# Optimization experiments

Measured on AMD Instinct MI355X. Metric: run time of the kernel, lower is better.

The kernel has to match this reference:

```python
import jax, jax.numpy as jnp
import numpy as np

EMBED = 128
HEADS = 32
HEAD_DIM = EMBED // HEADS  # 4
BATCH = 32
SEQ = 2048


def setup_inputs() -> dict:
    key = jax.random.key(0)
    ks = jax.random.split(key, 6)
    s = 1.0 / np.sqrt(EMBED)
    return {
        "x": jax.random.normal(ks[0], (BATCH, SEQ, EMBED), dtype=jnp.float32),
        # torch Linear weights are (out_features, in_features)
        "Wq": jax.random.uniform(ks[1], (EMBED, EMBED), jnp.float32, -s, s),
        "Wk": jax.random.uniform(ks[2], (EMBED, EMBED), jnp.float32, -s, s),
        "Wv": jax.random.uniform(ks[3], (EMBED, EMBED), jnp.float32, -s, s),
        "Wo": jax.random.uniform(ks[4], (EMBED, EMBED), jnp.float32, -s, s),
        "bo": jax.random.uniform(ks[5], (EMBED,), jnp.float32, -s, s),
    }


def reference(x, Wq, Wk, Wv, Wo, bo):
    b, s, e = x.shape
    h, d = HEADS, HEAD_DIM
    # projections (torch Linear: x @ W.T)
    q = (x @ Wq.T).reshape(b, s, h, d)
    k = (x @ Wk.T).reshape(b, s, h, d)
    v = (x @ Wv.T).reshape(b, s, h, d)
    # FAITHFUL to source: einsum 'bnqh,bnkh->bnqk' on (b, seq, heads, head_dim)
    # => n = seq position, q/k = HEADS. Attention is over the heads axis.
    scale = 1.0 / (float(d) ** 0.5)
    scores = jnp.einsum('bnqh,bnkh->bnqk', q, k) * scale  # (b, seq, heads, heads)
    attn = jax.nn.softmax(scores, axis=-1)
    attended = jnp.einsum('bnqk,bnkv->bnqv', attn, v).reshape(b, s, e)
    return attended @ Wo.T + bo
```

## Files before the change

kernel.cpp:

```cpp
#include <hip/hip_runtime.h>


#define TOKENS (32 * 2048)
#define E 128
#define NH 32
#define BT 16
#define THREADS 128
#define LPITCH 136

typedef __attribute__((ext_vector_type(4))) float f32x4;
typedef __attribute__((ext_vector_type(16))) float f32x16;
typedef __fp16 h8_t __attribute__((ext_vector_type(8)));

#if __has_builtin(__builtin_amdgcn_exp2f)
#define EXP2F __builtin_amdgcn_exp2f
#else
#define EXP2F exp2f
#endif

#if __has_builtin(__builtin_amdgcn_rcpf)
#define RCPF __builtin_amdgcn_rcpf
#else
#define RCPF(x) (1.0f / (x))
#endif

static __device__ __forceinline__ unsigned pk16(float a, float b) {
    return __builtin_bit_cast(unsigned, __builtin_amdgcn_cvt_pkrtz(a, b));
}

static __device__ __forceinline__ f32x16 zero16() {
    f32x16 z;
#pragma unroll
    for (int i = 0; i < 16; ++i) z[i] = 0.f;
    return z;
}

static __device__ __forceinline__ int vperm(int kh) {
    return ((kh >> 4) & 1) * 16 + ((kh >> 2) & 1) * 8 + ((kh >> 3) & 1) * 4 + (kh & 3);
}

__global__ void pack_w(const float* __restrict__ Wq, const float* __restrict__ Wk,
                       const float* __restrict__ Wv, const float* __restrict__ Wo,
                       __fp16* __restrict__ wpk) {
    int idx = blockIdx.x * blockDim.x + threadIdx.x;
    if (idx >= 4 * 8 * 4 * 64) return;
    int lane = idx & 63;
    int ks   = (idx >> 6) & 3;
    int nt   = (idx >> 8) & 7;
    int proj = idx >> 11;
    const float* W = (proj == 0) ? Wq : (proj == 1) ? Wk : (proj == 2) ? Wv : Wo;
    float scl = (proj == 1) ? 0.72134752044448170f : 1.0f;
    int c = lane & 15, g = lane >> 4;
    const float* src = W + (size_t)(nt * 16 + c) * E + ks * 32 + g * 8;
    __fp16* dst = wpk + (size_t)idx * 8;
#pragma unroll
    for (int j = 0; j < 8; ++j) dst[j] = (__fp16)(src[j] * scl);
}

__global__ __launch_bounds__(THREADS) void mha_fused(
        const float* __restrict__ x, const __fp16* __restrict__ wpk,
        const float* __restrict__ bo, float* __restrict__ out) {
    __shared__ __align__(16) __fp16 qs [BT * LPITCH];
    __shared__ __align__(16) __fp16 ksh[BT * LPITCH];
    __shared__ __align__(16) __fp16 vth[BT * LPITCH];

    const int tid  = threadIdx.x;
    const int wave = tid >> 6;
    const int lane = tid & 63;
    const int c = lane & 15, g = lane >> 4;
    const int bt0 = blockIdx.x * BT;

    {
        h8_t afrag[4];
        const float* xrow = x + (size_t)(bt0 + c) * E;
#pragma unroll
        for (int ks2 = 0; ks2 < 4; ++ks2) {
            const float* p = xrow + ks2 * 32 + g * 8;
            float4 v0 = *(const float4*)(p);
            float4 v1 = *(const float4*)(p + 4);
            uint4 au;
            au.x = pk16(v0.x, v0.y);
            au.y = pk16(v0.z, v0.w);
            au.z = pk16(v1.x, v1.y);
            au.w = pk16(v1.z, v1.w);
            afrag[ks2] = __builtin_bit_cast(h8_t, au);
        }

#pragma unroll
        for (int i = 0; i < 12; ++i) {
            int nc   = i * 2 + wave;
            int proj = i >> 2;
            int nt   = nc & 7;
            const __fp16* wb = wpk + ((size_t)((proj * 8 + nt) * 4) * 64 + lane) * 8;
            f32x4 acc = {0.f, 0.f, 0.f, 0.f};
#pragma unroll
            for (int ks2 = 0; ks2 < 4; ++ks2) {
                h8_t wf = *(const h8_t*)(wb + (size_t)ks2 * 64 * 8);
                acc = __builtin_amdgcn_mfma_f32_16x16x32_f16(wf, afrag[ks2], acc, 0, 0, 0);
            }
            if (proj < 2) {
                __fp16* dst = proj ? ksh : qs;
                uint2 st = make_uint2(pk16(acc[0], acc[1]), pk16(acc[2], acc[3]));
                *(uint2*)(dst + c * LPITCH + nt * 16 + g * 4) = st;
            } else {
                int vp = vperm(nt * 4 + g);
#pragma unroll
                for (int r2 = 0; r2 < 4; ++r2)
                    vth[c * LPITCH + r2 * 32 + vp] = (__fp16)acc[r2];
            }
        }
    }
    __syncthreads();

    {
        const int c32 = lane & 31;
        const int gg  = lane >> 5;
        const uint4 ONES4 = make_uint4(0x3C003C00u, 0x3C003C00u, 0x3C003C00u, 0x3C003C00u);
        const f32x16 z = zero16();
        const int tb = wave * 8;
#pragma unroll 1
        for (int pr = 0; pr < 4; ++pr) {
            const int t0 = tb + pr * 2, t1 = t0 + 1;
            const __fp16* v0r = vth + t0 * LPITCH;
            const __fp16* v1r = vth + t1 * LPITCH;

            uint4 ka0 = {0u,0u,0u,0u}, qa0 = {0u,0u,0u,0u};
            uint4 ka1 = {0u,0u,0u,0u}, qa1 = {0u,0u,0u,0u};
            if (gg == 0) {
                uint2 t;
                t = *(const uint2*)(ksh + t0 * LPITCH + c32 * 4); ka0.x = t.x; ka0.y = t.y;
                t = *(const uint2*)(qs  + t0 * LPITCH + c32 * 4); qa0.x = t.x; qa0.y = t.y;
                t = *(const uint2*)(ksh + t1 * LPITCH + c32 * 4); ka1.x = t.x; ka1.y = t.y;
                t = *(const uint2*)(qs  + t1 * LPITCH + c32 * 4); qa1.x = t.x; qa1.y = t.y;
            }
            uint4 va00 = *(const uint4*)(v0r + (c32 & 3) * 32 + gg * 8);
            uint4 va01 = *(const uint4*)(v0r + (c32 & 3) * 32 + 16 + gg * 8);
            uint4 va10 = *(const uint4*)(v1r + (c32 & 3) * 32 + gg * 8);
            uint4 va11 = *(const uint4*)(v1r + (c32 & 3) * 32 + 16 + gg * 8);
            if (c32 == 4) { va00 = ONES4; va01 = ONES4; va10 = ONES4; va11 = ONES4; }

            f32x16 sc0 = __builtin_amdgcn_mfma_f32_32x32x16_f16(
                __builtin_bit_cast(h8_t, ka0), __builtin_bit_cast(h8_t, qa0), z, 0, 0, 0);
            f32x16 sc1 = __builtin_amdgcn_mfma_f32_32x32x16_f16(
                __builtin_bit_cast(h8_t, ka1), __builtin_bit_cast(h8_t, qa1), z, 0, 0, 0);

            uint4 p00u, p01u, p10u, p11u;
            {
                float e[16];
#pragma unroll
                for (int r = 0; r < 16; ++r) e[r] = EXP2F(sc0[r]);
                p00u = make_uint4(pk16(e[0], e[1]),  pk16(e[2], e[3]),
                                  pk16(e[4], e[5]),  pk16(e[6], e[7]));
                p01u = make_uint4(pk16(e[8], e[9]),  pk16(e[10], e[11]),
                                  pk16(e[12], e[13]), pk16(e[14], e[15]));
            }
            {
                float e[16];
#pragma unroll
                for (int r = 0; r < 16; ++r) e[r] = EXP2F(sc1[r]);
                p10u = make_uint4(pk16(e[0], e[1]),  pk16(e[2], e[3]),
                                  pk16(e[4], e[5]),  pk16(e[6], e[7]));
                p11u = make_uint4(pk16(e[8], e[9]),  pk16(e[10], e[11]),
                                  pk16(e[12], e[13]), pk16(e[14], e[15]));
            }

            f32x16 pv0 = __builtin_amdgcn_mfma_f32_32x32x16_f16(
                __builtin_bit_cast(h8_t, va00), __builtin_bit_cast(h8_t, p00u), z, 0, 0, 0);
            pv0 = __builtin_amdgcn_mfma_f32_32x32x16_f16(
                __builtin_bit_cast(h8_t, va01), __builtin_bit_cast(h8_t, p01u), pv0, 0, 0, 0);
            f32x16 pv1 = __builtin_amdgcn_mfma_f32_32x32x16_f16(
                __builtin_bit_cast(h8_t, va10), __builtin_bit_cast(h8_t, p10u), z, 0, 0, 0);
            pv1 = __builtin_amdgcn_mfma_f32_32x32x16_f16(
                __builtin_bit_cast(h8_t, va11), __builtin_bit_cast(h8_t, p11u), pv1, 0, 0, 0);

            float s0 = __shfl(pv0[0], c32 + 32, 64);
            float s1 = __shfl(pv1[0], c32 + 32, 64);
            float r0 = RCPF(s0), r1 = RCPF(s1);
            if (lane < 32) {
                uint2 st0 = make_uint2(pk16(pv0[0] * r0, pv0[1] * r0),
                                       pk16(pv0[2] * r0, pv0[3] * r0));
                uint2 st1 = make_uint2(pk16(pv1[0] * r1, pv1[1] * r1),
                                       pk16(pv1[2] * r1, pv1[3] * r1));
                *(uint2*)(qs + t0 * LPITCH + c32 * 4) = st0;
                *(uint2*)(qs + t1 * LPITCH + c32 * 4) = st1;
            }
        }
    }
    __syncthreads();

    {
        h8_t af[4];
#pragma unroll
        for (int ks2 = 0; ks2 < 4; ++ks2) {
            af[ks2] = *(const h8_t*)(qs + c * LPITCH + ks2 * 32 + g * 8);
        }
#pragma unroll
        for (int i = 0; i < 4; ++i) {
            int nt = wave * 4 + i;
            const __fp16* wb = wpk + ((size_t)((3 * 8 + nt) * 4) * 64 + lane) * 8;
            f32x4 acc = {0.f, 0.f, 0.f, 0.f};
#pragma unroll
            for (int ks2 = 0; ks2 < 4; ++ks2) {
                h8_t b = *(const h8_t*)(wb + (size_t)ks2 * 64 * 8);
                acc = __builtin_amdgcn_mfma_f32_16x16x32_f16(b, af[ks2], acc, 0, 0, 0);
            }
            int col0 = nt * 16 + g * 4;
            float4 b4 = *(const float4*)(bo + col0);
            float4 st = make_float4(acc[0] + b4.x, acc[1] + b4.y,
                                    acc[2] + b4.z, acc[3] + b4.w);
            *(float4*)(out + (size_t)(bt0 + c) * E + col0) = st;
        }
    }
}

extern "C" void kernel_launch(void* const* d_in, const int* in_sizes, int n_in,
                              void* d_out, int out_size, void* d_ws, size_t ws_size,
                              hipStream_t stream) {
    const float* x  = (const float*)d_in[0];
    const float* Wq = (const float*)d_in[1];
    const float* Wk = (const float*)d_in[2];
    const float* Wv = (const float*)d_in[3];
    const float* Wo = (const float*)d_in[4];
    const float* bo = (const float*)d_in[5];
    __fp16* wpk = (__fp16*)d_ws;
    float* out = (float*)d_out;

    pack_w<<<32, 256, 0, stream>>>(Wq, Wk, Wv, Wo, wpk);
    mha_fused<<<TOKENS / BT, THREADS, 0, stream>>>(x, wpk, bo, out);
}
```

Baseline: 46.09 us.

## Process 64 tokens per block to reuse weight fragments across four token groups

Result: slower. 49.94 us (+8.3%).

```diff
diff --git a/kernel.cpp b/kernel.cpp
--- a/kernel.cpp
+++ b/kernel.cpp
@@ -4,7 +4,7 @@
 #define TOKENS (32 * 2048)
 #define E 128
 #define NH 32
-#define BT 16
+#define BT 64
 #define THREADS 128
 #define LPITCH 136
 
@@ -71,19 +71,22 @@
     const int bt0 = blockIdx.x * BT;
 
     {
-        h8_t afrag[4];
-        const float* xrow = x + (size_t)(bt0 + c) * E;
-#pragma unroll
-        for (int ks2 = 0; ks2 < 4; ++ks2) {
-            const float* p = xrow + ks2 * 32 + g * 8;
-            float4 v0 = *(const float4*)(p);
-            float4 v1 = *(const float4*)(p + 4);
-            uint4 au;
-            au.x = pk16(v0.x, v0.y);
-            au.y = pk16(v0.z, v0.w);
-            au.z = pk16(v1.x, v1.y);
-            au.w = pk16(v1.z, v1.w);
-            afrag[ks2] = __builtin_bit_cast(h8_t, au);
+        h8_t afrag[4][4];
+#pragma unroll
+        for (int tg = 0; tg < 4; ++tg) {
+            const float* xrow = x + (size_t)(bt0 + tg * 16 + c) * E;
+#pragma unroll
+            for (int ks2 = 0; ks2 < 4; ++ks2) {
+                const float* p = xrow + ks2 * 32 + g * 8;
+                float4 v0 = *(const float4*)(p);
+                float4 v1 = *(const float4*)(p + 4);
+                uint4 au;
+                au.x = pk16(v0.x, v0.y);
+                au.y = pk16(v0.z, v0.w);
+                au.z = pk16(v1.x, v1.y);
+                au.w = pk16(v1.z, v1.w);
+                afrag[tg][ks2] = __builtin_bit_cast(h8_t, au);
+            }
         }
 
 #pragma unroll
@@ -92,21 +95,27 @@
             int proj = i >> 2;
             int nt   = nc & 7;
             const __fp16* wb = wpk + ((size_t)((proj * 8 + nt) * 4) * 64 + lane) * 8;
-            f32x4 acc = {0.f, 0.f, 0.f, 0.f};
-#pragma unroll
-            for (int ks2 = 0; ks2 < 4; ++ks2) {
-                h8_t wf = *(const h8_t*)(wb + (size_t)ks2 * 64 * 8);
-                acc = __builtin_amdgcn_mfma_f32_16x16x32_f16(wf, afrag[ks2], acc, 0, 0, 0);
-            }
-            if (proj < 2) {
-                __fp16* dst = proj ? ksh : qs;
-                uint2 st = make_uint2(pk16(acc[0], acc[1]), pk16(acc[2], acc[3]));
-                *(uint2*)(dst + c * LPITCH + nt * 16 + g * 4) = st;
-            } else {
-                int vp = vperm(nt * 4 + g);
-#pragma unroll
-                for (int r2 = 0; r2 < 4; ++r2)
-                    vth[c * LPITCH + r2 * 32 + vp] = (__fp16)acc[r2];
+            h8_t wf[4];
+#pragma unroll
+            for (int ks2 = 0; ks2 < 4; ++ks2)
+                wf[ks2] = *(const h8_t*)(wb + (size_t)ks2 * 64 * 8);
+#pragma unroll
+            for (int tg = 0; tg < 4; ++tg) {
+                f32x4 acc = {0.f, 0.f, 0.f, 0.f};
+#pragma unroll
+                for (int ks2 = 0; ks2 < 4; ++ks2)
+                    acc = __builtin_amdgcn_mfma_f32_16x16x32_f16(wf[ks2], afrag[tg][ks2], acc, 0, 0, 0);
+                int tok = tg * 16 + c;
+                if (proj < 2) {
+                    __fp16* dst = proj ? ksh : qs;
+                    uint2 st = make_uint2(pk16(acc[0], acc[1]), pk16(acc[2], acc[3]));
+                    *(uint2*)(dst + tok * LPITCH + nt * 16 + g * 4) = st;
+                } else {
+                    int vp = vperm(nt * 4 + g);
+#pragma unroll
+                    for (int r2 = 0; r2 < 4; ++r2)
+                        vth[tok * LPITCH + r2 * 32 + vp] = (__fp16)acc[r2];
+                }
             }
         }
     }
@@ -117,9 +126,9 @@
         const int gg  = lane >> 5;
         const uint4 ONES4 = make_uint4(0x3C003C00u, 0x3C003C00u, 0x3C003C00u, 0x3C003C00u);
         const f32x16 z = zero16();
-        const int tb = wave * 8;
+        const int tb = wave * 32;
 #pragma unroll 1
-        for (int pr = 0; pr < 4; ++pr) {
+        for (int pr = 0; pr < 16; ++pr) {
             const int t0 = tb + pr * 2, t1 = t0 + 1;
             const __fp16* v0r = vth + t0 * LPITCH;
             const __fp16* v1r = vth + t1 * LPITCH;
@@ -189,26 +198,37 @@
     __syncthreads();
 
     {
-        h8_t af[4];
-#pragma unroll
-        for (int ks2 = 0; ks2 < 4; ++ks2) {
-            af[ks2] = *(const h8_t*)(qs + c * LPITCH + ks2 * 32 + g * 8);
-        }
+        h8_t wf[4][4];
 #pragma unroll
         for (int i = 0; i < 4; ++i) {
             int nt = wave * 4 + i;
             const __fp16* wb = wpk + ((size_t)((3 * 8 + nt) * 4) * 64 + lane) * 8;
-            f32x4 acc = {0.f, 0.f, 0.f, 0.f};
-#pragma unroll
-            for (int ks2 = 0; ks2 < 4; ++ks2) {
-                h8_t b = *(const h8_t*)(wb + (size_t)ks2 * 64 * 8);
-                acc = __builtin_amdgcn_mfma_f32_16x16x32_f16(b, af[ks2], acc, 0, 0, 0);
-            }
-            int col0 = nt * 16 + g * 4;
-            float4 b4 = *(const float4*)(bo + col0);
-            float4 st = make_float4(acc[0] + b4.x, acc[1] + b4.y,
-                                    acc[2] + b4.z, acc[3] + b4.w);
-            *(float4*)(out + (size_t)(bt0 + c) * E + col0) = st;
+#pragma unroll
+            for (int ks2 = 0; ks2 < 4; ++ks2)
+                wf[i][ks2] = *(const h8_t*)(wb + (size_t)ks2 * 64 * 8);
+        }
+        float4 b4[4];
+#pragma unroll
+        for (int i = 0; i < 4; ++i)
+            b4[i] = *(const float4*)(bo + (wave * 4 + i) * 16 + g * 4);
+
+#pragma unroll
+        for (int tg = 0; tg < 4; ++tg) {
+            h8_t af[4];
+#pragma unroll
+            for (int ks2 = 0; ks2 < 4; ++ks2)
+                af[ks2] = *(const h8_t*)(qs + (tg * 16 + c) * LPITCH + ks2 * 32 + g * 8);
+#pragma unroll
+            for (int i = 0; i < 4; ++i) {
+                f32x4 acc = {0.f, 0.f, 0.f, 0.f};
+#pragma unroll
+                for (int ks2 = 0; ks2 < 4; ++ks2)
+                    acc = __builtin_amdgcn_mfma_f32_16x16x32_f16(wf[i][ks2], af[ks2], acc, 0, 0, 0);
+                int col0 = (wave * 4 + i) * 16 + g * 4;
+                float4 st = make_float4(acc[0] + b4[i].x, acc[1] + b4[i].y,
+                                        acc[2] + b4[i].z, acc[3] + b4[i].w);
+                *(float4*)(out + (size_t)(bt0 + tg * 16 + c) * E + col0) = st;
+            }
         }
     }
 }
```

## Give each wave its own token tile to remove block-level barriers

Applied to the files above, without the earlier changes.

Result: faster. 42.17 us (-8.5%).

```diff
diff --git a/kernel.cpp b/kernel.cpp
--- a/kernel.cpp
+++ b/kernel.cpp
@@ -4,7 +4,7 @@
 #define TOKENS (32 * 2048)
 #define E 128
 #define NH 32
-#define BT 16
+#define WTOK 16
 #define THREADS 128
 #define LPITCH 136
 
@@ -60,19 +60,23 @@
 __global__ __launch_bounds__(THREADS) void mha_fused(
         const float* __restrict__ x, const __fp16* __restrict__ wpk,
         const float* __restrict__ bo, float* __restrict__ out) {
-    __shared__ __align__(16) __fp16 qs [BT * LPITCH];
-    __shared__ __align__(16) __fp16 ksh[BT * LPITCH];
-    __shared__ __align__(16) __fp16 vth[BT * LPITCH];
+    __shared__ __align__(16) __fp16 qs [2 * WTOK * LPITCH];
+    __shared__ __align__(16) __fp16 ksh[2 * WTOK * LPITCH];
+    __shared__ __align__(16) __fp16 vth[2 * WTOK * LPITCH];
 
     const int tid  = threadIdx.x;
     const int wave = tid >> 6;
     const int lane = tid & 63;
     const int c = lane & 15, g = lane >> 4;
-    const int bt0 = blockIdx.x * BT;
+    const int tbase = blockIdx.x * (2 * WTOK) + wave * WTOK;
+
+    __fp16* qsw = qs  + wave * WTOK * LPITCH;
+    __fp16* ksw = ksh + wave * WTOK * LPITCH;
+    __fp16* vtw = vth + wave * WTOK * LPITCH;
 
     {
         h8_t afrag[4];
-        const float* xrow = x + (size_t)(bt0 + c) * E;
+        const float* xrow = x + (size_t)(tbase + c) * E;
 #pragma unroll
         for (int ks2 = 0; ks2 < 4; ++ks2) {
             const float* p = xrow + ks2 * 32 + g * 8;
@@ -87,9 +91,8 @@
         }
 
 #pragma unroll
-        for (int i = 0; i < 12; ++i) {
-            int nc   = i * 2 + wave;
-            int proj = i >> 2;
+        for (int nc = 0; nc < 24; ++nc) {
+            int proj = nc >> 3;
             int nt   = nc & 7;
             const __fp16* wb = wpk + ((size_t)((proj * 8 + nt) * 4) * 64 + lane) * 8;
             f32x4 acc = {0.f, 0.f, 0.f, 0.f};
@@ -99,39 +102,37 @@
                 acc = __builtin_amdgcn_mfma_f32_16x16x32_f16(wf, afrag[ks2], acc, 0, 0, 0);
             }
             if (proj < 2) {
-                __fp16* dst = proj ? ksh : qs;
+                __fp16* dst = proj ? ksw : qsw;
                 uint2 st = make_uint2(pk16(acc[0], acc[1]), pk16(acc[2], acc[3]));
                 *(uint2*)(dst + c * LPITCH + nt * 16 + g * 4) = st;
             } else {
                 int vp = vperm(nt * 4 + g);
 #pragma unroll
                 for (int r2 = 0; r2 < 4; ++r2)
-                    vth[c * LPITCH + r2 * 32 + vp] = (__fp16)acc[r2];
+                    vtw[c * LPITCH + r2 * 32 + vp] = (__fp16)acc[r2];
             }
         }
     }
-    __syncthreads();
 
     {
         const int c32 = lane & 31;
         const int gg  = lane >> 5;
         const uint4 ONES4 = make_uint4(0x3C003C00u, 0x3C003C00u, 0x3C003C00u, 0x3C003C00u);
         const f32x16 z = zero16();
-        const int tb = wave * 8;
 #pragma unroll 1
-        for (int pr = 0; pr < 4; ++pr) {
-            const int t0 = tb + pr * 2, t1 = t0 + 1;
-            const __fp16* v0r = vth + t0 * LPITCH;
-            const __fp16* v1r = vth + t1 * LPITCH;
+        for (int pr = 0; pr < 8; ++pr) {
+            const int t0 = pr * 2, t1 = t0 + 1;
+            const __fp16* v0r = vtw + t0 * LPITCH;
+            const __fp16* v1r = vtw + t1 * LPITCH;
 
             uint4 ka0 = {0u,0u,0u,0u}, qa0 = {0u,0u,0u,0u};
             uint4 ka1 = {0u,0u,0u,0u}, qa1 = {0u,0u,0u,0u};
             if (gg == 0) {
                 uint2 t;
-                t = *(const uint2*)(ksh + t0 * LPITCH + c32 * 4); ka0.x = t.x; ka0.y = t.y;
-                t = *(const uint2*)(qs  + t0 * LPITCH + c32 * 4); qa0.x = t.x; qa0.y = t.y;
-                t = *(const uint2*)(ksh + t1 * LPITCH + c32 * 4); ka1.x = t.x; ka1.y = t.y;
-                t = *(const uint2*)(qs  + t1 * LPITCH + c32 * 4); qa1.x = t.x; qa1.y = t.y;
+                t = *(const uint2*)(ksw + t0 * LPITCH + c32 * 4); ka0.x = t.x; ka0.y = t.y;
+                t = *(const uint2*)(qsw + t0 * LPITCH + c32 * 4); qa0.x = t.x; qa0.y = t.y;
+                t = *(const uint2*)(ksw + t1 * LPITCH + c32 * 4); ka1.x = t.x; ka1.y = t.y;
+                t = *(const uint2*)(qsw + t1 * LPITCH + c32 * 4); qa1.x = t.x; qa1.y = t.y;
             }
             uint4 va00 = *(const uint4*)(v0r + (c32 & 3) * 32 + gg * 8);
             uint4 va01 = *(const uint4*)(v0r + (c32 & 3) * 32 + 16 + gg * 8);
@@ -181,22 +182,19 @@
                                        pk16(pv0[2] * r0, pv0[3] * r0));
                 uint2 st1 = make_uint2(pk16(pv1[0] * r1, pv1[1] * r1),
                                        pk16(pv1[2] * r1, pv1[3] * r1));
-                *(uint2*)(qs + t0 * LPITCH + c32 * 4) = st0;
-                *(uint2*)(qs + t1 * LPITCH + c32 * 4) = st1;
+                *(uint2*)(qsw + t0 * LPITCH + c32 * 4) = st0;
+                *(uint2*)(qsw + t1 * LPITCH + c32 * 4) = st1;
             }
         }
     }
-    __syncthreads();
 
     {
         h8_t af[4];
 #pragma unroll
-        for (int ks2 = 0; ks2 < 4; ++ks2) {
-            af[ks2] = *(const h8_t*)(qs + c * LPITCH + ks2 * 32 + g * 8);
-        }
-#pragma unroll
-        for (int i = 0; i < 4; ++i) {
-            int nt = wave * 4 + i;
+        for (int ks2 = 0; ks2 < 4; ++ks2)
+            af[ks2] = *(const h8_t*)(qsw + c * LPITCH + ks2 * 32 + g * 8);
+#pragma unroll
+        for (int nt = 0; nt < 8; ++nt) {
             const __fp16* wb = wpk + ((size_t)((3 * 8 + nt) * 4) * 64 + lane) * 8;
             f32x4 acc = {0.f, 0.f, 0.f, 0.f};
 #pragma unroll
@@ -208,7 +206,7 @@
             float4 b4 = *(const float4*)(bo + col0);
             float4 st = make_float4(acc[0] + b4.x, acc[1] + b4.y,
                                     acc[2] + b4.z, acc[3] + b4.w);
-            *(float4*)(out + (size_t)(bt0 + c) * E + col0) = st;
+            *(float4*)(out + (size_t)(tbase + c) * E + col0) = st;
         }
     }
 }
@@ -226,5 +224,5 @@
     float* out = (float*)d_out;
 
     pack_w<<<32, 256, 0, stream>>>(Wq, Wk, Wv, Wo, wpk);
-    mha_fused<<<TOKENS / BT, THREADS, 0, stream>>>(x, wpk, bo, out);
-}
+    mha_fused<<<TOKENS / (2 * WTOK), THREADS, 0, stream>>>(x, wpk, bo, out);
+}
```
